# Kernel optimization log

Hardware: AMD Instinct MI355X
Metric: run time of the kernel (lower is better)

Reference implementation:

```python
import jax, jax.numpy as jnp
import numpy as np

B, N, M, D = 4, 512, 512, 128
H, DOUT = 256, 128

def setup_inputs() -> dict:
    key = jax.random.key(0)
    k = jax.random.split(key, 4)
    X = jax.random.normal(k[0], (B, N, D), dtype=jnp.float32)
    Y = jax.random.normal(k[1], (B, M, D), dtype=jnp.float32)
    W1 = jax.random.normal(k[2], (2 * D, H), dtype=jnp.float32) / np.sqrt(2 * D)
    b1 = jnp.zeros((H,), dtype=jnp.float32)
    W2 = jax.random.normal(k[3], (H, DOUT), dtype=jnp.float32) / np.sqrt(H)
    b2 = jnp.zeros((DOUT,), dtype=jnp.float32)
    return {"X": X, "Y": Y, "W1": W1, "b1": b1, "W2": W2, "b2": b2}

def reference(X, Y, W1, b1, W2, b2):
    # pairs[b,n,m,:] = concat(Y[b,m], X[b,n])  -> [B,N,M,2D]
    n_ = X.shape[1]
    m_ = Y.shape[1]
    Ye = jnp.broadcast_to(Y[:, None, :, :], (X.shape[0], n_, m_, Y.shape[-1]))
    Xe = jnp.broadcast_to(X[:, :, None, :], (X.shape[0], n_, m_, X.shape[-1]))
    pairs = jnp.concatenate([Ye, Xe], axis=-1)
    # pointwise MLP: Linear -> ReLU -> Linear
    hdn = jax.nn.relu(jnp.einsum('bnmd,dh->bnmh', pairs, W1) + b1)
    Z = jnp.einsum('bnmh,ho->bnmo', hdn, W2) + b2
    # pool='sum' over the M (neighbor) dimension
    return jnp.sum(Z, axis=2)  # [B, N, DOUT]
```

## Files before the change

kernel.cpp:

```cpp
#include <hip/hip_runtime.h>

#define BB    4
#define NN    512
#define MM    512
#define DD    128
#define HH    256
#define DOUTC 128

typedef float v4f __attribute__((ext_vector_type(4)));

__device__ __forceinline__ v4f shfl_xor4(v4f v, int m) {
    v4f r;
    r.x = __shfl_xor(v.x, m, 64);
    r.y = __shfl_xor(v.y, m, 64);
    r.z = __shfl_xor(v.z, m, 64);
    r.w = __shfl_xor(v.w, m, 64);
    return r;
}

__global__ __launch_bounds__(1024) void precompute_ac(
    const float* __restrict__ X, const float* __restrict__ Y,
    const float* __restrict__ W1, const float* __restrict__ b1,
    float* __restrict__ AC)
{
    __shared__ __align__(16) float rows[16][DD];
    __shared__ __align__(16) v4f mrg[3][4][4][64];
    const int bid = blockIdx.x;
    const int t   = threadIdx.x;
    const int isC = bid >> 7;
    const int r0  = (bid & 127) * 16;
    const float* src = isC ? X : Y;

    if (t < 512)
        reinterpret_cast<v4f*>(&rows[0][0])[t] =
            reinterpret_cast<const v4f*>(src + (size_t)r0 * DD)[t];
    __syncthreads();

    const int hq = t & 63;
    const int dq = (t >> 6) & 3;
    const int rs = t >> 8;
    const int d0 = dq * 32;
    const float* wp = W1 + (isC ? DD * HH : 0) + hq * 4;

    v4f acc[4];
#pragma unroll
    for (int r = 0; r < 4; ++r) acc[r] = (v4f){0.f, 0.f, 0.f, 0.f};

#pragma unroll 2
    for (int dg = 0; dg < 32; dg += 4) {
        const int d = d0 + dg;
        const v4f w0 = *reinterpret_cast<const v4f*>(&wp[(d + 0) * HH]);
        const v4f w1 = *reinterpret_cast<const v4f*>(&wp[(d + 1) * HH]);
        const v4f w2 = *reinterpret_cast<const v4f*>(&wp[(d + 2) * HH]);
        const v4f w3 = *reinterpret_cast<const v4f*>(&wp[(d + 3) * HH]);
#pragma unroll
        for (int r = 0; r < 4; ++r) {
            const v4f rv = *reinterpret_cast<const v4f*>(&rows[rs * 4 + r][d]);
            acc[r] += w0 * rv.x;
            acc[r] += w1 * rv.y;
            acc[r] += w2 * rv.z;
            acc[r] += w3 * rv.w;
        }
    }

    if (dq > 0) {
#pragma unroll
        for (int r = 0; r < 4; ++r) mrg[dq - 1][rs][r][hq] = acc[r];
    }
    __syncthreads();
    if (dq == 0) {
#pragma unroll
        for (int r = 0; r < 4; ++r) {
#pragma unroll
            for (int p = 0; p < 3; ++p) acc[r] += mrg[p][rs][r][hq];
        }
        v4f bias = (v4f){0.f, 0.f, 0.f, 0.f};
        if (isC) bias = *reinterpret_cast<const v4f*>(&b1[hq * 4]);
#pragma unroll
        for (int r = 0; r < 4; ++r)
            *reinterpret_cast<v4f*>(
                &AC[((size_t)(isC * 2048 + r0 + rs * 4 + r)) * HH + hq * 4]) =
                acc[r] + bias;
    }
}

__global__ __launch_bounds__(1024) void fused_main(
    const float* __restrict__ A, const float* __restrict__ C,
    const float* __restrict__ W2, const float* __restrict__ b2,
    float* __restrict__ out)
{
    __shared__ __align__(16) v4f scratch[1536];
    __shared__ __align__(16) v4f satp[3][4][16];
    __shared__ __align__(16) float S[8][HH];
    const int bid = blockIdx.x;
    const int b   = (bid & 7) >> 1;
    const int n0  = ((((bid >> 3) << 1) | (bid & 1))) * 8;
    const int t   = threadIdx.x;

    const int w    = t >> 6;
    const int l    = t & 63;
    const int hg   = w & 3;
    const int qm   = w >> 2;
    const int hq   = l & 15;
    const int msub = l >> 4;
    const int h0   = hg * 64 + hq * 4;

    const float* Cb = C + ((size_t)(b * NN + n0)) * HH + h0;
    v4f c[8];
#pragma unroll
    for (int j = 0; j < 8; ++j)
        c[j] = *reinterpret_cast<const v4f*>(&Cb[(size_t)j * HH]);

    v4f acc[8], sat = (v4f){0.f, 0.f, 0.f, 0.f};
#pragma unroll
    for (int j = 0; j < 8; ++j) acc[j] = (v4f){0.f, 0.f, 0.f, 0.f};

    const float* Ab = A + ((size_t)(b * MM + qm * 128 + msub)) * HH + h0;
#pragma unroll 4
    for (int i = 0; i < 32; ++i) {
        const v4f a = *reinterpret_cast<const v4f*>(&Ab[(size_t)i * 4 * HH]);
        sat += a;
#pragma unroll
        for (int j = 0; j < 8; ++j) {
            const v4f s = a + c[j];
            acc[j].x += fabsf(s.x);
            acc[j].y += fabsf(s.y);
            acc[j].z += fabsf(s.z);
            acc[j].w += fabsf(s.w);
        }
    }

#pragma unroll
    for (int mask = 16; mask <= 32; mask <<= 1) {
#pragma unroll
        for (int j = 0; j < 8; ++j) acc[j] += shfl_xor4(acc[j], mask);
        sat += shfl_xor4(sat, mask);
    }

    if (qm > 0 && l < 16) {
#pragma unroll
        for (int j = 0; j < 8; ++j)
            scratch[(((qm - 1) * 4 + hg) * 8 + j) * 16 + l] = acc[j];
        satp[qm - 1][hg][l] = sat;
    }
    __syncthreads();

    if (qm == 0 && l < 16) {
#pragma unroll
        for (int p = 0; p < 3; ++p) {
#pragma unroll
            for (int j = 0; j < 8; ++j)
                acc[j] += scratch[((p * 4 + hg) * 8 + j) * 16 + l];
            sat += satp[p][hg][l];
        }
#pragma unroll
        for (int j = 0; j < 8; ++j) {
            const v4f sv = 0.5f * (sat + 512.f * c[j] + acc[j]);
            *reinterpret_cast<v4f*>(&S[j][h0]) = sv;
        }
    }
    __syncthreads();

    const int o0 = (t & 31) * 4;
    const int r  = (t >> 5) & 7;
    const int kq = t >> 8;
    const int k0 = kq * 64;
    v4f a4 = (v4f){0.f, 0.f, 0.f, 0.f};
    const float* w2p = W2 + o0;
#pragma unroll 4
    for (int k = k0; k < k0 + 64; k += 4) {
        const v4f sv = *reinterpret_cast<const v4f*>(&S[r][k]);
        const v4f wA = *reinterpret_cast<const v4f*>(&w2p[(k + 0) * DOUTC]);
        const v4f wB = *reinterpret_cast<const v4f*>(&w2p[(k + 1) * DOUTC]);
        const v4f wC = *reinterpret_cast<const v4f*>(&w2p[(k + 2) * DOUTC]);
        const v4f wD = *reinterpret_cast<const v4f*>(&w2p[(k + 3) * DOUTC]);
        a4 += wA * sv.x;
        a4 += wB * sv.y;
        a4 += wC * sv.z;
        a4 += wD * sv.w;
    }
    if (kq) scratch[(kq - 1) * 256 + (t & 255)] = a4;
    __syncthreads();
    if (kq == 0) {
#pragma unroll
        for (int p = 0; p < 3; ++p) a4 += scratch[p * 256 + t];
        a4 += 512.f * (*reinterpret_cast<const v4f*>(&b2[o0]));
        *reinterpret_cast<v4f*>(&out[((size_t)(b * NN + n0 + r)) * DOUTC + o0]) = a4;
    }
}

extern "C" void kernel_launch(void* const* d_in, const int* in_sizes, int n_in,
                              void* d_out, int out_size, void* d_ws, size_t ws_size,
                              hipStream_t stream) {
    const float* X  = (const float*)d_in[0];
    const float* Y  = (const float*)d_in[1];
    const float* W1 = (const float*)d_in[2];
    const float* b1 = (const float*)d_in[3];
    const float* W2 = (const float*)d_in[4];
    const float* b2 = (const float*)d_in[5];
    float* out = (float*)d_out;

    float* AC = (float*)d_ws;
    float* A  = AC;
    float* Cm = AC + 2048 * HH;

    hipLaunchKernelGGL(precompute_ac, dim3(256), dim3(1024), 0, stream,
                       X, Y, W1, b1, AC);
    hipLaunchKernelGGL(fused_main, dim3(256), dim3(1024), 0, stream,
                       A, Cm, W2, b2, out);
}
```

Baseline: 43.04 us.

## Restructure fused_main: 512 blocks of 512 threads, 4 rows each, packed v2f adds

Rebuilds the main kernel's work split. Each block now handles 4 output rows instead of 8, with 512 threads rather than 1024 and twice as many blocks. Each wave takes 64 contiguous M rows across the full H width, so the cross-lane shuffle reduction is gone and partials merge through shared memory over 8 waves. The abs-sum loop uses two-wide vector adds to encourage packed FP32 instructions. The trade-off is twice the A reads across blocks and a larger shared-memory merge.

```diff
diff --git a/kernel.cpp b/kernel.cpp
--- a/kernel.cpp
+++ b/kernel.cpp
@@ -7,16 +7,8 @@
 #define HH    256
 #define DOUTC 128
 
+typedef float v2f __attribute__((ext_vector_type(2)));
 typedef float v4f __attribute__((ext_vector_type(4)));
-
-__device__ __forceinline__ v4f shfl_xor4(v4f v, int m) {
-    v4f r;
-    r.x = __shfl_xor(v.x, m, 64);
-    r.y = __shfl_xor(v.y, m, 64);
-    r.z = __shfl_xor(v.z, m, 64);
-    r.w = __shfl_xor(v.w, m, 64);
-    return r;
-}
 
 __global__ __launch_bounds__(1024) void precompute_ac(
     const float* __restrict__ X, const float* __restrict__ Y,
@@ -84,86 +76,82 @@
     }
 }
 
-__global__ __launch_bounds__(1024) void fused_main(
+__global__ __launch_bounds__(512) void fused_main(
     const float* __restrict__ A, const float* __restrict__ C,
     const float* __restrict__ W2, const float* __restrict__ b2,
     float* __restrict__ out)
 {
-    __shared__ __align__(16) v4f scratch[1536];
-    __shared__ __align__(16) v4f satp[3][4][16];
-    __shared__ __align__(16) float S[8][HH];
+    __shared__ __align__(16) v4f mergeA[8][4][64];
+    __shared__ __align__(16) v4f mergeS[8][64];
+    __shared__ __align__(16) float S[4][HH];
     const int bid = blockIdx.x;
-    const int b   = (bid & 7) >> 1;
-    const int n0  = ((((bid >> 3) << 1) | (bid & 1))) * 8;
+    const int b   = bid >> 7;
+    const int n0  = (bid & 127) * 4;
     const int t   = threadIdx.x;
-
-    const int w    = t >> 6;
-    const int l    = t & 63;
-    const int hg   = w & 3;
-    const int qm   = w >> 2;
-    const int hq   = l & 15;
-    const int msub = l >> 4;
-    const int h0   = hg * 64 + hq * 4;
+    const int l   = t & 63;
+    const int qm  = t >> 6;
+    const int h0  = l * 4;
 
     const float* Cb = C + ((size_t)(b * NN + n0)) * HH + h0;
-    v4f c[8];
-#pragma unroll
-    for (int j = 0; j < 8; ++j)
-        c[j] = *reinterpret_cast<const v4f*>(&Cb[(size_t)j * HH]);
-
-    v4f acc[8], sat = (v4f){0.f, 0.f, 0.f, 0.f};
-#pragma unroll
-    for (int j = 0; j < 8; ++j) acc[j] = (v4f){0.f, 0.f, 0.f, 0.f};
-
-    const float* Ab = A + ((size_t)(b * MM + qm * 128 + msub)) * HH + h0;
+    v4f c4[4];
+#pragma unroll
+    for (int j = 0; j < 4; ++j)
+        c4[j] = *reinterpret_cast<const v4f*>(&Cb[(size_t)j * HH]);
+    v2f c01[4], c23[4];
+#pragma unroll
+    for (int j = 0; j < 4; ++j) {
+        c01[j] = (v2f){c4[j].x, c4[j].y};
+        c23[j] = (v2f){c4[j].z, c4[j].w};
+    }
+
+    float acc[4][4];
+#pragma unroll
+    for (int j = 0; j < 4; ++j)
+#pragma unroll
+        for (int u = 0; u < 4; ++u) acc[j][u] = 0.f;
+    v2f sat01 = (v2f){0.f, 0.f}, sat23 = (v2f){0.f, 0.f};
+
+    const float* Ab = A + ((size_t)(b * MM + qm * 64)) * HH + h0;
 #pragma unroll 4
-    for (int i = 0; i < 32; ++i) {
-        const v4f a = *reinterpret_cast<const v4f*>(&Ab[(size_t)i * 4 * HH]);
-        sat += a;
-#pragma unroll
-        for (int j = 0; j < 8; ++j) {
-            const v4f s = a + c[j];
-            acc[j].x += fabsf(s.x);
-            acc[j].y += fabsf(s.y);
-            acc[j].z += fabsf(s.z);
-            acc[j].w += fabsf(s.w);
+    for (int m = 0; m < 64; ++m) {
+        const v4f a = *reinterpret_cast<const v4f*>(&Ab[(size_t)m * HH]);
+        const v2f a01 = (v2f){a.x, a.y};
+        const v2f a23 = (v2f){a.z, a.w};
+        sat01 += a01;
+        sat23 += a23;
+#pragma unroll
+        for (int j = 0; j < 4; ++j) {
+            const v2f s01 = a01 + c01[j];
+            const v2f s23 = a23 + c23[j];
+            acc[j][0] += fabsf(s01.x);
+            acc[j][1] += fabsf(s01.y);
+            acc[j][2] += fabsf(s23.x);
+            acc[j][3] += fabsf(s23.y);
         }
     }
 
 #pragma unroll
-    for (int mask = 16; mask <= 32; mask <<= 1) {
-#pragma unroll
-        for (int j = 0; j < 8; ++j) acc[j] += shfl_xor4(acc[j], mask);
-        sat += shfl_xor4(sat, mask);
-    }
-
-    if (qm > 0 && l < 16) {
-#pragma unroll
-        for (int j = 0; j < 8; ++j)
-            scratch[(((qm - 1) * 4 + hg) * 8 + j) * 16 + l] = acc[j];
-        satp[qm - 1][hg][l] = sat;
-    }
-    __syncthreads();
-
-    if (qm == 0 && l < 16) {
-#pragma unroll
-        for (int p = 0; p < 3; ++p) {
-#pragma unroll
-            for (int j = 0; j < 8; ++j)
-                acc[j] += scratch[((p * 4 + hg) * 8 + j) * 16 + l];
-            sat += satp[p][hg][l];
-        }
-#pragma unroll
-        for (int j = 0; j < 8; ++j) {
-            const v4f sv = 0.5f * (sat + 512.f * c[j] + acc[j]);
-            *reinterpret_cast<v4f*>(&S[j][h0]) = sv;
-        }
+    for (int j = 0; j < 4; ++j)
+        mergeA[qm][j][l] = (v4f){acc[j][0], acc[j][1], acc[j][2], acc[j][3]};
+    mergeS[qm][l] = (v4f){sat01.x, sat01.y, sat23.x, sat23.y};
+    __syncthreads();
+
+    if (qm < 4) {
+        const int r = qm;
+        v4f sum = mergeA[0][r][l];
+#pragma unroll
+        for (int p = 1; p < 8; ++p) sum += mergeA[p][r][l];
+        v4f st = mergeS[0][l];
+#pragma unroll
+        for (int p = 1; p < 8; ++p) st += mergeS[p][l];
+        const v4f sval = 0.5f * (st + 512.f * c4[r] + sum);
+        *reinterpret_cast<v4f*>(&S[r][h0]) = sval;
     }
     __syncthreads();
 
     const int o0 = (t & 31) * 4;
-    const int r  = (t >> 5) & 7;
-    const int kq = t >> 8;
+    const int r  = (t >> 5) & 3;
+    const int kq = t >> 7;
     const int k0 = kq * 64;
     v4f a4 = (v4f){0.f, 0.f, 0.f, 0.f};
     const float* w2p = W2 + o0;
@@ -179,11 +167,12 @@
         a4 += wC * sv.z;
         a4 += wD * sv.w;
     }
-    if (kq) scratch[(kq - 1) * 256 + (t & 255)] = a4;
+    v4f* red = reinterpret_cast<v4f*>(&mergeA[0][0][0]);
+    if (kq) red[(kq - 1) * 128 + (t & 127)] = a4;
     __syncthreads();
     if (kq == 0) {
 #pragma unroll
-        for (int p = 0; p < 3; ++p) a4 += scratch[p * 256 + t];
+        for (int p = 0; p < 3; ++p) a4 += red[p * 128 + (t & 127)];
         a4 += 512.f * (*reinterpret_cast<const v4f*>(&b2[o0]));
         *reinterpret_cast<v4f*>(&out[((size_t)(b * NN + n0 + r)) * DOUTC + o0]) = a4;
     }
@@ -206,6 +195,6 @@
 
     hipLaunchKernelGGL(precompute_ac, dim3(256), dim3(1024), 0, stream,
                        X, Y, W1, b1, AC);
-    hipLaunchKernelGGL(fused_main, dim3(256), dim3(1024), 0, stream,
+    hipLaunchKernelGGL(fused_main, dim3(512), dim3(512), 0, stream,
                        A, Cm, W2, b2, out);
 }
```

Measured after the change: 42.29 us. Within noise of the previous version (-1.7%).
